# Optimization experiments

Measured on AMD Instinct MI355X. Metric: run time of the kernel, lower is better.

Reference implementation:

```python
import jax, jax.numpy as jnp
import numpy as np

B, S, H, NH = 8, 2048, 128, 4
HS = H // NH
EPS = 1e-8


def setup_inputs() -> dict:
    key = jax.random.key(0)
    ks = jax.random.split(key, 20)
    sc = 1.0 / np.sqrt(H)
    d = {
        'item_embeds': jax.random.normal(ks[0], (B, S, H), jnp.float32),
        'behavior_embeds': jax.random.normal(ks[1], (B, S, H), jnp.float32),
        'attn_mask': jnp.zeros((B, 1, S, S), jnp.float32),
    }
    names = ['Wq', 'Wk', 'Wv', 'Wqb', 'Wkb', 'Wvb', 'Wf']
    for i, n in enumerate(names):
        d[n] = jax.random.normal(ks[2 + i], (H, H), jnp.float32) * sc
        d['b' + n[1:]] = jnp.zeros((H,), jnp.float32)
    d['ln_w'] = jnp.ones((H,), jnp.float32)
    d['ln_b'] = jnp.zeros((H,), jnp.float32)
    return d


def _split_heads(x):
    # [B,S,H] -> [B,NH,S,HS]
    return x.reshape(B, S, NH, HS).transpose(0, 2, 1, 3)


def _layer_norm(x, w, b):
    u = jnp.mean(x, -1, keepdims=True)
    s = jnp.mean((x - u) ** 2, -1, keepdims=True)
    return w * ((x - u) / jnp.sqrt(s + EPS)) + b


def reference(item_embeds, behavior_embeds, attn_mask,
              Wq, bq, Wk, bk, Wv, bv,
              Wqb, bqb, Wkb, bkb, Wvb, bvb,
              Wf, bf, ln_w, ln_b):
    Q = _split_heads(item_embeds @ Wq + bq)
    K = _split_heads(item_embeds @ Wk + bk)
    V = _split_heads(item_embeds @ Wv + bv)
    Qb = _split_heads(behavior_embeds @ Wqb + bqb)
    Kb = _split_heads(behavior_embeds @ Wkb + bkb)
    # V_behavior computed in the original forward but unused downstream
    _Vb = _split_heads(behavior_embeds @ Wvb + bvb)
    scores = (jnp.einsum('bhqd,bhkd->bhqk', Q, K)
              + jnp.einsum('bhqd,bhkd->bhqk', Qb, Kb)) / np.sqrt(HS)
    scores = scores + attn_mask
    probs = jax.nn.softmax(scores, axis=-1)
    attn_out = jnp.einsum('bhqk,bhkd->bhqd', probs, V)
    attn_out = attn_out.transpose(0, 2, 1, 3).reshape(B, S, H)
    out = attn_out @ Wf + bf
    return _layer_norm(out + item_embeds, ln_w, ln_b)
```

## Files before the change

### kernel.cpp

```cpp
#include <hip/hip_runtime.h>
#include <math.h>

typedef unsigned short ushort_t;
typedef __attribute__((ext_vector_type(8))) short bf16x8;
typedef __attribute__((ext_vector_type(4))) float f32x4;

namespace {
constexpr int B = 8, S = 2048, H = 128, NH = 4, HS = 32;
constexpr float EPS = 1e-8f;
constexpr float SCALE = 0.17677669529663687f;
constexpr int QT = 16, KT = 64;
constexpr int NE = B * S * H;
}

__device__ __forceinline__ ushort_t f2bf(float f) {
  unsigned u = __float_as_uint(f);
  unsigned r = (u + 0x7FFFu + ((u >> 16) & 1u)) >> 16;
  return (ushort_t)r;
}

__device__ __forceinline__ f32x4 mfma16(bf16x8 a, bf16x8 b, f32x4 c) {
  return __builtin_amdgcn_mfma_f32_16x16x32_bf16(a, b, c, 0, 0, 0);
}

__global__ __launch_bounds__(256) void wcvt_kernel(
    const float* __restrict__ Wq, const float* __restrict__ Wk, const float* __restrict__ Wv,
    const float* __restrict__ Wqb, const float* __restrict__ Wkb, const float* __restrict__ Wf,
    ushort_t* __restrict__ Wt)
{
  const float* Ws[6] = {Wq, Wk, Wv, Wqb, Wkb, Wf};
  const float scl[6] = {SCALE, 1.f, 1.f, SCALE, 1.f, 1.f};
  const int m = blockIdx.y;
  const int kb = blockIdx.x;
  const float* W = Ws[m];
  const float sc = scl[m];
  __shared__ float T[32 * 132];
  const int t = threadIdx.x;
#pragma unroll
  for (int u = 0; u < 4; ++u) {
    const int idx = u * 256 + t;
    const int row = idx >> 5, c4 = idx & 31;
    const float4 v = *(const float4*)&W[(kb * 32 + row) * H + c4 * 4];
    *(float4*)&T[row * 132 + c4 * 4] = v;
  }
  __syncthreads();
#pragma unroll
  for (int u = 0; u < 16; ++u) {
    const int idx = u * 256 + t;
    const int n = idx >> 5, kk = idx & 31;
    Wt[m * (H * H) + n * H + kb * 32 + kk] = f2bf(T[kk * 132 + n] * sc);
  }
}

__global__ __launch_bounds__(256) void proj_kernel(
    const float* __restrict__ item, const float* __restrict__ beh,
    const ushort_t* __restrict__ Wt,
    const float* __restrict__ bq, const float* __restrict__ bk, const float* __restrict__ bv,
    const float* __restrict__ bqb, const float* __restrict__ bkb,
    ushort_t* __restrict__ Qo, ushort_t* __restrict__ Ko, ushort_t* __restrict__ Qbo,
    ushort_t* __restrict__ Kbo, ushort_t* __restrict__ Vto)
{
  __shared__ ushort_t Xi[32 * 136];
  __shared__ ushort_t Xb[32 * 136];
  __shared__ ushort_t Yb[32 * 136];
  const int t = threadIdx.x;
  const long r0 = (long)blockIdx.x * 32;
#pragma unroll
  for (int u = 0; u < 4; ++u) {
    const int idx = u * 256 + t;
    const int row = idx >> 5, c4 = idx & 31;
    const float4 vi = *(const float4*)&item[(r0 + row) * H + c4 * 4];
    const float4 vb = *(const float4*)&beh[(r0 + row) * H + c4 * 4];
    unsigned long long pi = (unsigned long long)f2bf(vi.x) | ((unsigned long long)f2bf(vi.y) << 16)
        | ((unsigned long long)f2bf(vi.z) << 32) | ((unsigned long long)f2bf(vi.w) << 48);
    unsigned long long pb = (unsigned long long)f2bf(vb.x) | ((unsigned long long)f2bf(vb.y) << 16)
        | ((unsigned long long)f2bf(vb.z) << 32) | ((unsigned long long)f2bf(vb.w) << 48);
    *(unsigned long long*)&Xi[row * 136 + c4 * 4] = pi;
    *(unsigned long long*)&Xb[row * 136 + c4 * 4] = pb;
  }
  __syncthreads();

  const int w = t >> 6, l = t & 63, l15 = l & 15, quad = l >> 4;
  const int bb = (int)(r0 >> 11);
  const int s0 = (int)(r0 & (S - 1));
  const float* bias[5] = {bq, bk, bv, bqb, bkb};
  const float bscale[5] = {SCALE, 1.f, 1.f, SCALE, 1.f};
  ushort_t* dsts[5] = {Qo, Ko, Vto, Qbo, Kbo};

  bf16x8 afi[2][4], afb[2][4];
#pragma unroll
  for (int mt = 0; mt < 2; ++mt)
#pragma unroll
    for (int ks = 0; ks < 4; ++ks) {
      afi[mt][ks] = *(const bf16x8*)&Xi[(mt * 16 + l15) * 136 + ks * 32 + quad * 8];
      afb[mt][ks] = *(const bf16x8*)&Xb[(mt * 16 + l15) * 136 + ks * 32 + quad * 8];
    }

  for (int p = 0; p < 5; ++p) {
    f32x4 acc[2][2];
#pragma unroll
    for (int nt = 0; nt < 2; ++nt) {
      const float bcol = bias[p][w * 32 + nt * 16 + l15] * bscale[p];
#pragma unroll
      for (int mt = 0; mt < 2; ++mt)
        acc[mt][nt] = (f32x4){bcol, bcol, bcol, bcol};
    }
    const ushort_t* Wp = Wt + p * (H * H);
    const bf16x8 (*af)[4] = (p < 3) ? afi : afb;
#pragma unroll
    for (int ks = 0; ks < 4; ++ks) {
      bf16x8 bfr[2];
#pragma unroll
      for (int nt = 0; nt < 2; ++nt)
        bfr[nt] = *(const bf16x8*)&Wp[(w * 32 + nt * 16 + l15) * H + ks * 32 + quad * 8];
#pragma unroll
      for (int mt = 0; mt < 2; ++mt)
#pragma unroll
        for (int nt = 0; nt < 2; ++nt)
          acc[mt][nt] = mfma16(af[mt][ks], bfr[nt], acc[mt][nt]);
    }
#pragma unroll
    for (int mt = 0; mt < 2; ++mt)
#pragma unroll
      for (int nt = 0; nt < 2; ++nt)
#pragma unroll
        for (int r = 0; r < 4; ++r)
          Yb[(mt * 16 + quad * 4 + r) * 136 + w * 32 + nt * 16 + l15] = f2bf(acc[mt][nt][r]);
    __syncthreads();
    ushort_t* dst = dsts[p];
    if (p == 2) {
      const int d = t >> 1, sh = (t & 1) * 16;
      ushort_t tmp[16];
#pragma unroll
      for (int i = 0; i < 16; ++i) tmp[i] = Yb[(sh + i) * 136 + d];
      const long gidx = ((long)(bb * NH + (d >> 5)) * HS + (d & 31)) * S + s0 + sh;
      *(uint4*)&dst[gidx] = *(const uint4*)&tmp[0];
      *(uint4*)&dst[gidx + 8] = *(const uint4*)&tmp[8];
    } else {
      const int row = t >> 3, cb = (t & 7) * 16;
      const int h = cb >> 5, dd = cb & 31;
      const long gidx = ((long)(bb * NH + h) * S + s0 + row) * HS + dd;
      *(uint4*)&dst[gidx] = *(const uint4*)&Yb[row * 136 + cb];
      *(uint4*)&dst[gidx + 8] = *(const uint4*)&Yb[row * 136 + cb + 8];
    }
    __syncthreads();
  }
}

__global__ __launch_bounds__(256, 4) void attn_kernel(
    const ushort_t* __restrict__ Q, const ushort_t* __restrict__ K,
    const ushort_t* __restrict__ Qb, const ushort_t* __restrict__ Kb,
    const ushort_t* __restrict__ Vt, const float* __restrict__ mask,
    ushort_t* __restrict__ attn_out)
{
  __shared__ ushort_t Pb[NH][16 * 72];
  const int t = threadIdx.x;
  const int w = t >> 6;
  const int l = t & 63, l15 = l & 15, quad = l >> 4;
  const int q0 = blockIdx.x * QT;
  const int b = blockIdx.y;
  const long hQ = (long)(b * NH + w) * S * HS;
  const long hV = (long)(b * NH + w) * HS * S;

  const bf16x8 qf  = *(const bf16x8*)&Q[hQ + (long)(q0 + l15) * HS + quad * 8];
  const bf16x8 qbf = *(const bf16x8*)&Qb[hQ + (long)(q0 + l15) * HS + quad * 8];

  const float* mrow[4];
#pragma unroll
  for (int r = 0; r < 4; ++r)
    mrow[r] = mask + ((long)b * S + q0 + quad * 4 + r) * S + l15;

  float mold[4], lsum[4];
  f32x4 O[2];
#pragma unroll
  for (int r = 0; r < 4; ++r) { mold[r] = -1e30f; lsum[r] = 0.f; }
#pragma unroll
  for (int dt = 0; dt < 2; ++dt) O[dt] = (f32x4){0.f, 0.f, 0.f, 0.f};
  ushort_t* Pw = Pb[w];

  for (int kt = 0; kt < S / KT; ++kt) {
    const int k0 = kt * KT;
    f32x4 sc[4];
#pragma unroll
    for (int nt = 0; nt < 4; ++nt)
#pragma unroll
      for (int r = 0; r < 4; ++r)
        sc[nt][r] = mrow[r][k0 + nt * 16];
    bf16x8 kf[4], kbf[4], vf[2][2];
#pragma unroll
    for (int nt = 0; nt < 4; ++nt) {
      kf[nt]  = *(const bf16x8*)&K[hQ + (long)(k0 + nt * 16 + l15) * HS + quad * 8];
      kbf[nt] = *(const bf16x8*)&Kb[hQ + (long)(k0 + nt * 16 + l15) * HS + quad * 8];
    }
#pragma unroll
    for (int dt = 0; dt < 2; ++dt)
#pragma unroll
      for (int ks = 0; ks < 2; ++ks)
        vf[dt][ks] = *(const bf16x8*)&Vt[hV + (long)(dt * 16 + l15) * S + k0 + ks * 32 + quad * 8];
#pragma unroll
    for (int nt = 0; nt < 4; ++nt) {
      sc[nt] = mfma16(qbf, kbf[nt], sc[nt]);
      sc[nt] = mfma16(qf, kf[nt], sc[nt]);
    }
    float alpha[4];
#pragma unroll
    for (int r = 0; r < 4; ++r) {
      float rm = fmaxf(fmaxf(sc[0][r], sc[1][r]), fmaxf(sc[2][r], sc[3][r]));
      rm = fmaxf(rm, __shfl_xor(rm, 1));
      rm = fmaxf(rm, __shfl_xor(rm, 2));
      rm = fmaxf(rm, __shfl_xor(rm, 4));
      rm = fmaxf(rm, __shfl_xor(rm, 8));
      const float mnew = fmaxf(mold[r], rm);
      alpha[r] = __expf(mold[r] - mnew);
      float rs = 0.f;
#pragma unroll
      for (int nt = 0; nt < 4; ++nt) {
        const float p = __expf(sc[nt][r] - mnew);
        sc[nt][r] = p;
        rs += p;
      }
      rs += __shfl_xor(rs, 1);
      rs += __shfl_xor(rs, 2);
      rs += __shfl_xor(rs, 4);
      rs += __shfl_xor(rs, 8);
      lsum[r] = lsum[r] * alpha[r] + rs;
      mold[r] = mnew;
    }
#pragma unroll
    for (int dt = 0; dt < 2; ++dt)
#pragma unroll
      for (int r = 0; r < 4; ++r)
        O[dt][r] *= alpha[r];
#pragma unroll
    for (int nt = 0; nt < 4; ++nt)
#pragma unroll
      for (int r = 0; r < 4; ++r)
        Pw[(quad * 4 + r) * 72 + nt * 16 + l15] = f2bf(sc[nt][r]);
    bf16x8 pf[2];
#pragma unroll
    for (int ks = 0; ks < 2; ++ks)
      pf[ks] = *(const bf16x8*)&Pw[l15 * 72 + ks * 32 + quad * 8];
#pragma unroll
    for (int dt = 0; dt < 2; ++dt)
#pragma unroll
      for (int ks = 0; ks < 2; ++ks)
        O[dt] = mfma16(pf[ks], vf[dt][ks], O[dt]);
  }
#pragma unroll
  for (int r = 0; r < 4; ++r) {
    const float inv = 1.f / lsum[r];
    const long row = (long)b * S + q0 + quad * 4 + r;
#pragma unroll
    for (int dt = 0; dt < 2; ++dt)
      attn_out[row * H + w * 32 + dt * 16 + l15] = f2bf(O[dt][r] * inv);
  }
}

__global__ __launch_bounds__(256) void out_kernel(
    const ushort_t* __restrict__ attn, const float* __restrict__ item,
    const ushort_t* __restrict__ Wft, const float* __restrict__ bf_,
    const float* __restrict__ lnw, const float* __restrict__ lnb,
    float* __restrict__ out)
{
  __shared__ ushort_t As[32 * 136];
  __shared__ float Ys[32 * 132];
  const int t = threadIdx.x;
  const long r0 = (long)blockIdx.x * 32;
#pragma unroll
  for (int u = 0; u < 2; ++u) {
    const int idx = u * 256 + t;
    const int row = idx >> 4, c8 = idx & 15;
    *(uint4*)&As[row * 136 + c8 * 8] = *(const uint4*)&attn[(r0 + row) * H + c8 * 8];
  }
  __syncthreads();
  const int w = t >> 6, l = t & 63, l15 = l & 15, quad = l >> 4;
  f32x4 acc[2][2];
#pragma unroll
  for (int nt = 0; nt < 2; ++nt) {
    const float bcol = bf_[w * 32 + nt * 16 + l15];
#pragma unroll
    for (int mt = 0; mt < 2; ++mt)
      acc[mt][nt] = (f32x4){bcol, bcol, bcol, bcol};
  }
#pragma unroll
  for (int ks = 0; ks < 4; ++ks) {
    bf16x8 bfr[2];
#pragma unroll
    for (int nt = 0; nt < 2; ++nt)
      bfr[nt] = *(const bf16x8*)&Wft[(w * 32 + nt * 16 + l15) * H + ks * 32 + quad * 8];
#pragma unroll
    for (int mt = 0; mt < 2; ++mt) {
      const bf16x8 a = *(const bf16x8*)&As[(mt * 16 + l15) * 136 + ks * 32 + quad * 8];
#pragma unroll
      for (int nt = 0; nt < 2; ++nt)
        acc[mt][nt] = mfma16(a, bfr[nt], acc[mt][nt]);
    }
  }
#pragma unroll
  for (int mt = 0; mt < 2; ++mt)
#pragma unroll
    for (int nt = 0; nt < 2; ++nt)
#pragma unroll
      for (int r = 0; r < 4; ++r) {
        const int rl = mt * 16 + quad * 4 + r;
        const int col = w * 32 + nt * 16 + l15;
        Ys[rl * 132 + col] = acc[mt][nt][r] + item[(r0 + rl) * H + col];
      }
  __syncthreads();
  const int rl = t >> 3, ch = t & 7;
  float v[16];
#pragma unroll
  for (int g = 0; g < 4; ++g) {
    const float4 y = *(const float4*)&Ys[rl * 132 + ch * 16 + g * 4];
    v[g * 4 + 0] = y.x; v[g * 4 + 1] = y.y; v[g * 4 + 2] = y.z; v[g * 4 + 3] = y.w;
  }
  float s = 0.f;
#pragma unroll
  for (int i = 0; i < 16; ++i) s += v[i];
  s += __shfl_xor(s, 1);
  s += __shfl_xor(s, 2);
  s += __shfl_xor(s, 4);
  const float u_ = s * (1.f / H);
  float s2 = 0.f;
#pragma unroll
  for (int i = 0; i < 16; ++i) { const float d = v[i] - u_; s2 += d * d; }
  s2 += __shfl_xor(s2, 1);
  s2 += __shfl_xor(s2, 2);
  s2 += __shfl_xor(s2, 4);
  const float rinv = rsqrtf(s2 * (1.f / H) + EPS);
#pragma unroll
  for (int g = 0; g < 4; ++g) {
    float4 o;
    const int col = ch * 16 + g * 4;
    o.x = lnw[col + 0] * ((v[g * 4 + 0] - u_) * rinv) + lnb[col + 0];
    o.y = lnw[col + 1] * ((v[g * 4 + 1] - u_) * rinv) + lnb[col + 1];
    o.z = lnw[col + 2] * ((v[g * 4 + 2] - u_) * rinv) + lnb[col + 2];
    o.w = lnw[col + 3] * ((v[g * 4 + 3] - u_) * rinv) + lnb[col + 3];
    *(float4*)&out[(r0 + rl) * H + col] = o;
  }
}

extern "C" void kernel_launch(void* const* d_in, const int* in_sizes, int n_in,
                              void* d_out, int out_size, void* d_ws, size_t ws_size,
                              hipStream_t stream) {
  const float* item = (const float*)d_in[0];
  const float* beh  = (const float*)d_in[1];
  const float* mask = (const float*)d_in[2];
  const float* Wq  = (const float*)d_in[3];  const float* bq  = (const float*)d_in[4];
  const float* Wk  = (const float*)d_in[5];  const float* bk  = (const float*)d_in[6];
  const float* Wv  = (const float*)d_in[7];  const float* bv  = (const float*)d_in[8];
  const float* Wqb = (const float*)d_in[9];  const float* bqb = (const float*)d_in[10];
  const float* Wkb = (const float*)d_in[11]; const float* bkb = (const float*)d_in[12];
  const float* Wf  = (const float*)d_in[15]; const float* bfv = (const float*)d_in[16];
  const float* lnw = (const float*)d_in[17]; const float* lnb = (const float*)d_in[18];
  float* out = (float*)d_out;

  ushort_t* ws = (ushort_t*)d_ws;
  ushort_t* Qw   = ws;
  ushort_t* Kw   = Qw + NE;
  ushort_t* Qbw  = Kw + NE;
  ushort_t* Kbw  = Qbw + NE;
  ushort_t* Vtw  = Kbw + NE;
  ushort_t* Attw = Vtw + NE;
  ushort_t* Wt   = Attw + NE;

  wcvt_kernel<<<dim3(4, 6), 256, 0, stream>>>(Wq, Wk, Wv, Wqb, Wkb, Wf, Wt);
  proj_kernel<<<dim3((B * S) / 32), 256, 0, stream>>>(
      item, beh, Wt, bq, bk, bv, bqb, bkb, Qw, Kw, Qbw, Kbw, Vtw);
  attn_kernel<<<dim3(S / QT, B), 256, 0, stream>>>(
      Qw, Kw, Qbw, Kbw, Vtw, mask, Attw);
  out_kernel<<<dim3((B * S) / 32), 256, 0, stream>>>(
      Attw, item, Wt + 5 * H * H, bfv, lnw, lnb, out);
}
```

Baseline: 378.4 us.

## Split attention keys across two wave halves and widen proj/out kernel grids

The attention kernel now runs 512 threads per block. Each head gets two waves that each handle half of the key range, and their partial softmax statistics (max, sum, output) are merged through shared memory. The projection kernel puts the five projections on a second grid dimension instead of looping over them in one block. The output kernel uses 16-row tiles instead of 32. These changes add parallelism and occupancy in every stage, at the cost of loading each input more than once in proj and an extra shared-memory merge step in attention.

```diff
diff --git a/kernel.cpp b/kernel.cpp
--- a/kernel.cpp
+++ b/kernel.cpp
@@ -60,23 +60,20 @@
     ushort_t* __restrict__ Qo, ushort_t* __restrict__ Ko, ushort_t* __restrict__ Qbo,
     ushort_t* __restrict__ Kbo, ushort_t* __restrict__ Vto)
 {
-  __shared__ ushort_t Xi[32 * 136];
-  __shared__ ushort_t Xb[32 * 136];
+  __shared__ ushort_t Xs[32 * 136];
   __shared__ ushort_t Yb[32 * 136];
   const int t = threadIdx.x;
+  const int p = blockIdx.y;
   const long r0 = (long)blockIdx.x * 32;
+  const float* X = (p < 3) ? item : beh;
 #pragma unroll
   for (int u = 0; u < 4; ++u) {
     const int idx = u * 256 + t;
     const int row = idx >> 5, c4 = idx & 31;
-    const float4 vi = *(const float4*)&item[(r0 + row) * H + c4 * 4];
-    const float4 vb = *(const float4*)&beh[(r0 + row) * H + c4 * 4];
-    unsigned long long pi = (unsigned long long)f2bf(vi.x) | ((unsigned long long)f2bf(vi.y) << 16)
-        | ((unsigned long long)f2bf(vi.z) << 32) | ((unsigned long long)f2bf(vi.w) << 48);
-    unsigned long long pb = (unsigned long long)f2bf(vb.x) | ((unsigned long long)f2bf(vb.y) << 16)
-        | ((unsigned long long)f2bf(vb.z) << 32) | ((unsigned long long)f2bf(vb.w) << 48);
-    *(unsigned long long*)&Xi[row * 136 + c4 * 4] = pi;
-    *(unsigned long long*)&Xb[row * 136 + c4 * 4] = pb;
+    const float4 v = *(const float4*)&X[(r0 + row) * H + c4 * 4];
+    unsigned long long pk = (unsigned long long)f2bf(v.x) | ((unsigned long long)f2bf(v.y) << 16)
+        | ((unsigned long long)f2bf(v.z) << 32) | ((unsigned long long)f2bf(v.w) << 48);
+    *(unsigned long long*)&Xs[row * 136 + c4 * 4] = pk;
   }
   __syncthreads();
 
@@ -87,80 +84,78 @@
   const float bscale[5] = {SCALE, 1.f, 1.f, SCALE, 1.f};
   ushort_t* dsts[5] = {Qo, Ko, Vto, Qbo, Kbo};
 
-  bf16x8 afi[2][4], afb[2][4];
+  bf16x8 af[2][4];
 #pragma unroll
   for (int mt = 0; mt < 2; ++mt)
 #pragma unroll
-    for (int ks = 0; ks < 4; ++ks) {
-      afi[mt][ks] = *(const bf16x8*)&Xi[(mt * 16 + l15) * 136 + ks * 32 + quad * 8];
-      afb[mt][ks] = *(const bf16x8*)&Xb[(mt * 16 + l15) * 136 + ks * 32 + quad * 8];
-    }
-
-  for (int p = 0; p < 5; ++p) {
-    f32x4 acc[2][2];
-#pragma unroll
-    for (int nt = 0; nt < 2; ++nt) {
-      const float bcol = bias[p][w * 32 + nt * 16 + l15] * bscale[p];
-#pragma unroll
-      for (int mt = 0; mt < 2; ++mt)
-        acc[mt][nt] = (f32x4){bcol, bcol, bcol, bcol};
-    }
-    const ushort_t* Wp = Wt + p * (H * H);
-    const bf16x8 (*af)[4] = (p < 3) ? afi : afb;
-#pragma unroll
-    for (int ks = 0; ks < 4; ++ks) {
-      bf16x8 bfr[2];
+    for (int ks = 0; ks < 4; ++ks)
+      af[mt][ks] = *(const bf16x8*)&Xs[(mt * 16 + l15) * 136 + ks * 32 + quad * 8];
+
+  f32x4 acc[2][2];
+#pragma unroll
+  for (int nt = 0; nt < 2; ++nt) {
+    const float bcol = bias[p][w * 32 + nt * 16 + l15] * bscale[p];
+#pragma unroll
+    for (int mt = 0; mt < 2; ++mt)
+      acc[mt][nt] = (f32x4){bcol, bcol, bcol, bcol};
+  }
+  const ushort_t* Wp = Wt + p * (H * H);
+#pragma unroll
+  for (int ks = 0; ks < 4; ++ks) {
+    bf16x8 bfr[2];
+#pragma unroll
+    for (int nt = 0; nt < 2; ++nt)
+      bfr[nt] = *(const bf16x8*)&Wp[(w * 32 + nt * 16 + l15) * H + ks * 32 + quad * 8];
+#pragma unroll
+    for (int mt = 0; mt < 2; ++mt)
 #pragma unroll
       for (int nt = 0; nt < 2; ++nt)
-        bfr[nt] = *(const bf16x8*)&Wp[(w * 32 + nt * 16 + l15) * H + ks * 32 + quad * 8];
-#pragma unroll
-      for (int mt = 0; mt < 2; ++mt)
-#pragma unroll
-        for (int nt = 0; nt < 2; ++nt)
-          acc[mt][nt] = mfma16(af[mt][ks], bfr[nt], acc[mt][nt]);
-    }
-#pragma unroll
-    for (int mt = 0; mt < 2; ++mt)
-#pragma unroll
-      for (int nt = 0; nt < 2; ++nt)
-#pragma unroll
-        for (int r = 0; r < 4; ++r)
-          Yb[(mt * 16 + quad * 4 + r) * 136 + w * 32 + nt * 16 + l15] = f2bf(acc[mt][nt][r]);
-    __syncthreads();
-    ushort_t* dst = dsts[p];
-    if (p == 2) {
-      const int d = t >> 1, sh = (t & 1) * 16;
-      ushort_t tmp[16];
-#pragma unroll
-      for (int i = 0; i < 16; ++i) tmp[i] = Yb[(sh + i) * 136 + d];
-      const long gidx = ((long)(bb * NH + (d >> 5)) * HS + (d & 31)) * S + s0 + sh;
-      *(uint4*)&dst[gidx] = *(const uint4*)&tmp[0];
-      *(uint4*)&dst[gidx + 8] = *(const uint4*)&tmp[8];
-    } else {
-      const int row = t >> 3, cb = (t & 7) * 16;
-      const int h = cb >> 5, dd = cb & 31;
-      const long gidx = ((long)(bb * NH + h) * S + s0 + row) * HS + dd;
-      *(uint4*)&dst[gidx] = *(const uint4*)&Yb[row * 136 + cb];
-      *(uint4*)&dst[gidx + 8] = *(const uint4*)&Yb[row * 136 + cb + 8];
-    }
-    __syncthreads();
-  }
-}
-
-__global__ __launch_bounds__(256, 4) void attn_kernel(
+        acc[mt][nt] = mfma16(af[mt][ks], bfr[nt], acc[mt][nt]);
+  }
+#pragma unroll
+  for (int mt = 0; mt < 2; ++mt)
+#pragma unroll
+    for (int nt = 0; nt < 2; ++nt)
+#pragma unroll
+      for (int r = 0; r < 4; ++r)
+        Yb[(mt * 16 + quad * 4 + r) * 136 + w * 32 + nt * 16 + l15] = f2bf(acc[mt][nt][r]);
+  __syncthreads();
+  ushort_t* dst = dsts[p];
+  if (p == 2) {
+    const int d = t >> 1, sh = (t & 1) * 16;
+    ushort_t tmp[16];
+#pragma unroll
+    for (int i = 0; i < 16; ++i) tmp[i] = Yb[(sh + i) * 136 + d];
+    const long gidx = ((long)(bb * NH + (d >> 5)) * HS + (d & 31)) * S + s0 + sh;
+    *(uint4*)&dst[gidx] = *(const uint4*)&tmp[0];
+    *(uint4*)&dst[gidx + 8] = *(const uint4*)&tmp[8];
+  } else {
+    const int row = t >> 3, cb = (t & 7) * 16;
+    const int h = cb >> 5, dd = cb & 31;
+    const long gidx = ((long)(bb * NH + h) * S + s0 + row) * HS + dd;
+    *(uint4*)&dst[gidx] = *(const uint4*)&Yb[row * 136 + cb];
+    *(uint4*)&dst[gidx + 8] = *(const uint4*)&Yb[row * 136 + cb + 8];
+  }
+}
+
+__global__ __launch_bounds__(512, 8) void attn_kernel(
     const ushort_t* __restrict__ Q, const ushort_t* __restrict__ K,
     const ushort_t* __restrict__ Qb, const ushort_t* __restrict__ Kb,
     const ushort_t* __restrict__ Vt, const float* __restrict__ mask,
     ushort_t* __restrict__ attn_out)
 {
-  __shared__ ushort_t Pb[NH][16 * 72];
+  __shared__ ushort_t Pb[8][16 * 72];
+  __shared__ float Ob[8][16][33];
+  __shared__ float Mb[8][16];
+  __shared__ float Lb[8][16];
   const int t = threadIdx.x;
   const int w = t >> 6;
+  const int head = w & 3, half = w >> 2;
   const int l = t & 63, l15 = l & 15, quad = l >> 4;
   const int q0 = blockIdx.x * QT;
   const int b = blockIdx.y;
-  const long hQ = (long)(b * NH + w) * S * HS;
-  const long hV = (long)(b * NH + w) * HS * S;
+  const long hQ = (long)(b * NH + head) * S * HS;
+  const long hV = (long)(b * NH + head) * HS * S;
 
   const bf16x8 qf  = *(const bf16x8*)&Q[hQ + (long)(q0 + l15) * HS + quad * 8];
   const bf16x8 qbf = *(const bf16x8*)&Qb[hQ + (long)(q0 + l15) * HS + quad * 8];
@@ -178,7 +173,8 @@
   for (int dt = 0; dt < 2; ++dt) O[dt] = (f32x4){0.f, 0.f, 0.f, 0.f};
   ushort_t* Pw = Pb[w];
 
-  for (int kt = 0; kt < S / KT; ++kt) {
+  const int kt0 = half * (S / KT / 2), kt1 = kt0 + (S / KT / 2);
+  for (int kt = kt0; kt < kt1; ++kt) {
     const int k0 = kt * KT;
     f32x4 sc[4];
 #pragma unroll
@@ -247,12 +243,34 @@
         O[dt] = mfma16(pf[ks], vf[dt][ks], O[dt]);
   }
 #pragma unroll
-  for (int r = 0; r < 4; ++r) {
-    const float inv = 1.f / lsum[r];
-    const long row = (long)b * S + q0 + quad * 4 + r;
-#pragma unroll
-    for (int dt = 0; dt < 2; ++dt)
-      attn_out[row * H + w * 32 + dt * 16 + l15] = f2bf(O[dt][r] * inv);
+  for (int dt = 0; dt < 2; ++dt)
+#pragma unroll
+    for (int r = 0; r < 4; ++r)
+      Ob[w][quad * 4 + r][dt * 16 + l15] = O[dt][r];
+  if (l15 == 0) {
+#pragma unroll
+    for (int r = 0; r < 4; ++r) {
+      Mb[w][quad * 4 + r] = mold[r];
+      Lb[w][quad * 4 + r] = lsum[r];
+    }
+  }
+  __syncthreads();
+  if (w < 4) {
+#pragma unroll
+    for (int r = 0; r < 4; ++r) {
+      const int rl = quad * 4 + r;
+      const float m1 = Mb[w][rl], m2 = Mb[w + 4][rl];
+      const float M = fmaxf(m1, m2);
+      const float w1 = __expf(m1 - M), w2 = __expf(m2 - M);
+      const float inv = 1.f / (Lb[w][rl] * w1 + Lb[w + 4][rl] * w2);
+      const long row = (long)b * S + q0 + rl;
+#pragma unroll
+      for (int dt = 0; dt < 2; ++dt) {
+        const int col = dt * 16 + l15;
+        const float o = Ob[w][rl][col] * w1 + Ob[w + 4][rl][col] * w2;
+        attn_out[row * H + w * 32 + col] = f2bf(o * inv);
+      }
+    }
   }
 }
 
@@ -262,76 +280,67 @@
     const float* __restrict__ lnw, const float* __restrict__ lnb,
     float* __restrict__ out)
 {
-  __shared__ ushort_t As[32 * 136];
-  __shared__ float Ys[32 * 132];
+  __shared__ ushort_t As[16 * 136];
+  __shared__ float Ys[16 * 132];
   const int t = threadIdx.x;
-  const long r0 = (long)blockIdx.x * 32;
-#pragma unroll
-  for (int u = 0; u < 2; ++u) {
-    const int idx = u * 256 + t;
-    const int row = idx >> 4, c8 = idx & 15;
+  const long r0 = (long)blockIdx.x * 16;
+  {
+    const int row = t >> 4, c8 = t & 15;
     *(uint4*)&As[row * 136 + c8 * 8] = *(const uint4*)&attn[(r0 + row) * H + c8 * 8];
   }
   __syncthreads();
   const int w = t >> 6, l = t & 63, l15 = l & 15, quad = l >> 4;
-  f32x4 acc[2][2];
+  f32x4 acc[2];
 #pragma unroll
   for (int nt = 0; nt < 2; ++nt) {
     const float bcol = bf_[w * 32 + nt * 16 + l15];
-#pragma unroll
-    for (int mt = 0; mt < 2; ++mt)
-      acc[mt][nt] = (f32x4){bcol, bcol, bcol, bcol};
+    acc[nt] = (f32x4){bcol, bcol, bcol, bcol};
   }
 #pragma unroll
   for (int ks = 0; ks < 4; ++ks) {
-    bf16x8 bfr[2];
-#pragma unroll
-    for (int nt = 0; nt < 2; ++nt)
-      bfr[nt] = *(const bf16x8*)&Wft[(w * 32 + nt * 16 + l15) * H + ks * 32 + quad * 8];
-#pragma unroll
-    for (int mt = 0; mt < 2; ++mt) {
-      const bf16x8 a = *(const bf16x8*)&As[(mt * 16 + l15) * 136 + ks * 32 + quad * 8];
-#pragma unroll
-      for (int nt = 0; nt < 2; ++nt)
-        acc[mt][nt] = mfma16(a, bfr[nt], acc[mt][nt]);
-    }
-  }
-#pragma unroll
-  for (int mt = 0; mt < 2; ++mt)
-#pragma unroll
-    for (int nt = 0; nt < 2; ++nt)
-#pragma unroll
-      for (int r = 0; r < 4; ++r) {
-        const int rl = mt * 16 + quad * 4 + r;
-        const int col = w * 32 + nt * 16 + l15;
-        Ys[rl * 132 + col] = acc[mt][nt][r] + item[(r0 + rl) * H + col];
-      }
-  __syncthreads();
-  const int rl = t >> 3, ch = t & 7;
-  float v[16];
-#pragma unroll
-  for (int g = 0; g < 4; ++g) {
-    const float4 y = *(const float4*)&Ys[rl * 132 + ch * 16 + g * 4];
+    const bf16x8 a = *(const bf16x8*)&As[l15 * 136 + ks * 32 + quad * 8];
+#pragma unroll
+    for (int nt = 0; nt < 2; ++nt) {
+      const bf16x8 bfr = *(const bf16x8*)&Wft[(w * 32 + nt * 16 + l15) * H + ks * 32 + quad * 8];
+      acc[nt] = mfma16(a, bfr, acc[nt]);
+    }
+  }
+#pragma unroll
+  for (int nt = 0; nt < 2; ++nt)
+#pragma unroll
+    for (int r = 0; r < 4; ++r) {
+      const int rl = quad * 4 + r;
+      const int col = w * 32 + nt * 16 + l15;
+      Ys[rl * 132 + col] = acc[nt][r] + item[(r0 + rl) * H + col];
+    }
+  __syncthreads();
+  const int rl = t >> 4, ch = t & 15;
+  float v[8];
+#pragma unroll
+  for (int g = 0; g < 2; ++g) {
+    const float4 y = *(const float4*)&Ys[rl * 132 + ch * 8 + g * 4];
     v[g * 4 + 0] = y.x; v[g * 4 + 1] = y.y; v[g * 4 + 2] = y.z; v[g * 4 + 3] = y.w;
   }
   float s = 0.f;
 #pragma unroll
-  for (int i = 0; i < 16; ++i) s += v[i];
+  for (int i = 0; i < 8; ++i) s += v[i];
   s += __shfl_xor(s, 1);
   s += __shfl_xor(s, 2);
   s += __shfl_xor(s, 4);
+  s += __shfl_xor(s, 8);
   const float u_ = s * (1.f / H);
   float s2 = 0.f;
 #pragma unroll
-  for (int i = 0; i < 16; ++i) { const float d = v[i] - u_; s2 += d * d; }
+  for (int i = 0; i < 8; ++i) { const float d = v[i] - u_; s2 += d * d; }
   s2 += __shfl_xor(s2, 1);
   s2 += __shfl_xor(s2, 2);
   s2 += __shfl_xor(s2, 4);
+  s2 += __shfl_xor(s2, 8);
   const float rinv = rsqrtf(s2 * (1.f / H) + EPS);
 #pragma unroll
-  for (int g = 0; g < 4; ++g) {
+  for (int g = 0; g < 2; ++g) {
     float4 o;
-    const int col = ch * 16 + g * 4;
+    const int col = ch * 8 + g * 4;
     o.x = lnw[col + 0] * ((v[g * 4 + 0] - u_) * rinv) + lnb[col + 0];
     o.y = lnw[col + 1] * ((v[g * 4 + 1] - u_) * rinv) + lnb[col + 1];
     o.z = lnw[col + 2] * ((v[g * 4 + 2] - u_) * rinv) + lnb[col + 2];
@@ -365,10 +374,10 @@
   ushort_t* Wt   = Attw + NE;
 
   wcvt_kernel<<<dim3(4, 6), 256, 0, stream>>>(Wq, Wk, Wv, Wqb, Wkb, Wf, Wt);
-  proj_kernel<<<dim3((B * S) / 32), 256, 0, stream>>>(
+  proj_kernel<<<dim3((B * S) / 32, 5), 256, 0, stream>>>(
       item, beh, Wt, bq, bk, bv, bqb, bkb, Qw, Kw, Qbw, Kbw, Vtw);
-  attn_kernel<<<dim3(S / QT, B), 256, 0, stream>>>(
+  attn_kernel<<<dim3(S / QT, B), 512, 0, stream>>>(
       Qw, Kw, Qbw, Kbw, Vtw, mask, Attw);
-  out_kernel<<<dim3((B * S) / 32), 256, 0, stream>>>(
+  out_kernel<<<dim3((B * S) / 16), 256, 0, stream>>>(
       Attw, item, Wt + 5 * H * H, bfv, lnw, lnb, out);
 }
```

After: 471.2 us. 1.25x slower.
